# Optimization experiments

Hardware: AMD Instinct MI355X
Metric: run time of the kernel (lower is better)

The kernel has to match this reference:

```python
import jax, jax.numpy as jnp
import numpy as np

B, N_LOCAL, N_GLOBAL, N_PLANE = 8, 512, 512, 512
LQ, LK, NUM_HEADS = 8192, 8192, 8


def setup_inputs() -> dict:
    key = jax.random.key(0)
    ks = jax.random.split(key, 6)
    s = 1.0 / np.sqrt(N_PLANE).astype(np.float32)
    return {
        "x_local": jax.random.normal(ks[0], (B, N_LOCAL, LQ), jnp.float32),
        "x_global": jax.random.normal(ks[1], (B, N_GLOBAL, LK), jnp.float32),
        "Wq": jax.random.normal(ks[2], (N_PLANE, N_LOCAL), jnp.float32) * s,
        "Wk": jax.random.normal(ks[3], (N_PLANE, N_GLOBAL), jnp.float32) * s,
        "Wv": jax.random.normal(ks[4], (N_PLANE, N_GLOBAL), jnp.float32) * s,
        "Wo": jax.random.normal(ks[5], (N_LOCAL, N_PLANE), jnp.float32) * s,
    }


def reference(x_local, x_global, Wq, Wk, Wv, Wo):
    # 1x1 Conv1d (bias=False) == channel-wise GEMM.
    b, _, lq = x_local.shape
    lk = x_global.shape[2]
    h = NUM_HEADS
    d = Wq.shape[0] // h  # d_k = n_plane // num_heads

    # project and split heads: [B, L, P] -> [B, H, L, d]
    q = jnp.einsum('pc,bcl->blp', Wq, x_local).reshape(b, lq, h, d).transpose(0, 2, 1, 3)
    k = jnp.einsum('pc,bcl->blp', Wk, x_global).reshape(b, lk, h, d).transpose(0, 2, 1, 3)
    v = jnp.einsum('pc,bcl->blp', Wv, x_global).reshape(b, lk, h, d).transpose(0, 2, 1, 3)

    # No softmax between QK^T and V -> reassociate: (Q @ K^T) @ V == Q @ (K^T @ V).
    # Avoids the O(Lq*Lk) logits tensor; mathematically identical.
    kv = jnp.einsum('bhkd,bhke->bhde', k, v)          # [B, H, d, d]
    out = jnp.einsum('bhld,bhde->bhle', q, kv) / d     # scale by d_k (as in source)

    # merge heads: [B, H, Lq, d] -> [B, Lq, P] -> output 1x1 conv -> [B, n_local, Lq]
    out = out.transpose(0, 2, 1, 3).reshape(b, lq, h * d)
    return jnp.einsum('op,blp->bol', Wo, out)
```

## Files before the change

kernel.cpp:

```cpp
#include <hip/hip_runtime.h>
#include <stdint.h>


typedef __attribute__((ext_vector_type(8))) short bf16x8;
typedef __attribute__((ext_vector_type(4))) float f32x4;

__device__ __forceinline__ short f2bf(float f) {
  union { float f; uint32_t u; } v; v.f = f;
  uint32_t r = v.u + 0x7FFFu + ((v.u >> 16) & 1u);
  return (short)(r >> 16);
}

__device__ __forceinline__ void async_ld16(const void* g, void* l) {
  __builtin_amdgcn_global_load_lds(
      (const __attribute__((address_space(1))) void*)g,
      (__attribute__((address_space(3))) void*)l, 16, 0, 0);
}

__launch_bounds__(256)
__global__ void prep_weights(const float* __restrict__ Wq, const float* __restrict__ Wk,
                             const float* __restrict__ Wv, const float* __restrict__ Wo,
                             short* __restrict__ Wqt, short* __restrict__ Wkb,
                             short* __restrict__ Wvb, short* __restrict__ Wob) {
  int i = blockIdx.x * 256 + threadIdx.x;
  Wkb[i] = f2bf(Wk[i]);
  Wvb[i] = f2bf(Wv[i]);
  Wob[i] = f2bf(Wo[i]);
  int c = i >> 9, p = i & 511;
  Wqt[i] = f2bf(Wq[p * 512 + c]);
}

__launch_bounds__(256)
__global__ void transpose_cast(const float* __restrict__ X, short* __restrict__ Xt) {
  __shared__ float tile[64][65];
  const int b = blockIdx.z;
  const int l0 = blockIdx.x * 64, c0 = blockIdx.y * 64;
  const int tx = threadIdx.x & 63, ty = threadIdx.x >> 6;
  const float* Xb = X + (size_t)b * 512 * 8192;
  short* Xtb = Xt + (size_t)b * 512 * 8192;
#pragma unroll
  for (int i = 0; i < 16; i++) {
    int c = ty * 16 + i;
    tile[c][tx] = Xb[(size_t)(c0 + c) * 8192 + l0 + tx];
  }
  __syncthreads();
#pragma unroll
  for (int i = 0; i < 16; i++) {
    int l = ty * 16 + i;
    Xtb[(size_t)(l0 + l) * 512 + c0 + tx] = f2bf(tile[tx][l]);
  }
}

template <bool OUT_BF16, bool A_BATCH>
__launch_bounds__(256)
__global__ void gemm_bt(const short* __restrict__ A, const short* __restrict__ B,
                        void* __restrict__ C, int M, int N, int K) {
  __shared__ __align__(16) short As[128 * 32];
  __shared__ __align__(16) short Bs[128 * 32];
  const int tid = threadIdx.x;
  const int lane = tid & 63;
  const int w = tid >> 6;
  const int wy = w >> 1, wx = w & 1;
  const int m0 = blockIdx.y * 128, n0 = blockIdx.x * 128;
  const size_t b = blockIdx.z;
  const short* Ab = A + (A_BATCH ? b * (size_t)M * K : (size_t)0);
  const short* Bb = B + b * (size_t)N * K;
  const int fr = lane & 15, fkg = lane >> 4;

  f32x4 acc[4][4] = {};

  for (int kk = 0; kk < K; kk += 32) {
    __syncthreads();
#pragma unroll
    for (int j = 0; j < 2; j++) {
      int ci = j * 256 + w * 64 + lane;
      int row = ci >> 2;
      int co = (ci & 3) * 8;
      async_ld16(Ab + (size_t)(m0 + row) * K + kk + co, &As[(j * 256 + w * 64) * 8]);
      async_ld16(Bb + (size_t)(n0 + row) * K + kk + co, &Bs[(j * 256 + w * 64) * 8]);
    }
    __syncthreads();

    bf16x8 af[4], bf[4];
#pragma unroll
    for (int t = 0; t < 4; t++) {
      af[t] = *(const bf16x8*)&As[(wy * 64 + t * 16 + fr) * 32 + fkg * 8];
      bf[t] = *(const bf16x8*)&Bs[(wx * 64 + t * 16 + fr) * 32 + fkg * 8];
    }
#pragma unroll
    for (int mt = 0; mt < 4; mt++)
#pragma unroll
      for (int nt = 0; nt < 4; nt++)
        acc[mt][nt] =
            __builtin_amdgcn_mfma_f32_16x16x32_bf16(af[mt], bf[nt], acc[mt][nt], 0, 0, 0);
  }

  const size_t cbase = b * (size_t)M * N;
#pragma unroll
  for (int mt = 0; mt < 4; mt++) {
#pragma unroll
    for (int nt = 0; nt < 4; nt++) {
      int n = n0 + wx * 64 + nt * 16 + fr;
#pragma unroll
      for (int r = 0; r < 4; r++) {
        int m = m0 + wy * 64 + mt * 16 + fkg * 4 + r;
        float v = acc[mt][nt][r];
        if (OUT_BF16)
          ((short*)C)[cbase + (size_t)m * N + n] = f2bf(v);
        else
          ((float*)C)[cbase + (size_t)m * N + n] = v;
      }
    }
  }
}

__launch_bounds__(256)
__global__ void kv_accum(const short* __restrict__ Kb, const short* __restrict__ Vb,
                         float* __restrict__ kv) {
  const int lane = threadIdx.x & 63, w = threadIdx.x >> 6;
  const int b = blockIdx.z, h = blockIdx.y;
  const int l0 = blockIdx.x * 2048 + w * 512;
  const short* Kh = Kb + ((size_t)b * 512 + h * 64) * 8192 + l0;
  const short* Vh = Vb + ((size_t)b * 512 + h * 64) * 8192 + l0;
  const int fr = lane & 15, fkg = lane >> 4;
  f32x4 acc[4][4] = {};
  for (int kk = 0; kk < 512; kk += 32) {
    bf16x8 af[4], bf[4];
#pragma unroll
    for (int t = 0; t < 4; t++) {
      af[t] = *(const bf16x8*)&Kh[(size_t)(t * 16 + fr) * 8192 + kk + fkg * 8];
      bf[t] = *(const bf16x8*)&Vh[(size_t)(t * 16 + fr) * 8192 + kk + fkg * 8];
    }
#pragma unroll
    for (int mt = 0; mt < 4; mt++)
#pragma unroll
      for (int nt = 0; nt < 4; nt++)
        acc[mt][nt] =
            __builtin_amdgcn_mfma_f32_16x16x32_bf16(af[mt], bf[nt], acc[mt][nt], 0, 0, 0);
  }
  float* kvb = kv + ((size_t)b * 8 + h) * 4096;
#pragma unroll
  for (int mt = 0; mt < 4; mt++)
#pragma unroll
    for (int nt = 0; nt < 4; nt++)
#pragma unroll
      for (int r = 0; r < 4; r++) {
        int d = mt * 16 + fkg * 4 + r, e = nt * 16 + fr;
        atomicAdd(&kvb[d * 64 + e], acc[mt][nt][r]);
      }
}

__launch_bounds__(256)
__global__ void u_compute(const float* __restrict__ kv, const short* __restrict__ Wqt,
                          short* __restrict__ Ut) {
  const int lane = threadIdx.x & 63, w = threadIdx.x >> 6;
  const int h = blockIdx.x, b = blockIdx.y;
  const float* kvb = kv + ((size_t)b * 8 + h) * 4096;
  const int fr = lane & 15, fkg = lane >> 4;
  f32x4 acc[4][8] = {};
#pragma unroll
  for (int ks = 0; ks < 2; ks++) {
    bf16x8 af[4];
#pragma unroll
    for (int mt = 0; mt < 4; mt++) {
      union { short s[8]; bf16x8 v; } u;
#pragma unroll
      for (int j = 0; j < 8; j++) {
        int d = ks * 32 + fkg * 8 + j;
        int e = mt * 16 + fr;
        u.s[j] = f2bf(kvb[d * 64 + e] * 0.015625f);
      }
      af[mt] = u.v;
    }
#pragma unroll
    for (int nt = 0; nt < 8; nt++) {
      int c = w * 128 + nt * 16 + fr;
      bf16x8 bfr = *(const bf16x8*)&Wqt[(size_t)c * 512 + h * 64 + ks * 32 + fkg * 8];
#pragma unroll
      for (int mt = 0; mt < 4; mt++)
        acc[mt][nt] =
            __builtin_amdgcn_mfma_f32_16x16x32_bf16(af[mt], bfr, acc[mt][nt], 0, 0, 0);
    }
  }
  short* Utb = Ut + (size_t)b * 262144;
#pragma unroll
  for (int mt = 0; mt < 4; mt++)
#pragma unroll
    for (int nt = 0; nt < 8; nt++) {
      int c = w * 128 + nt * 16 + fr;
#pragma unroll
      for (int r = 0; r < 4; r++) {
        int e = mt * 16 + fkg * 4 + r;
        Utb[(size_t)c * 512 + h * 64 + e] = f2bf(acc[mt][nt][r]);
      }
    }
}

extern "C" void kernel_launch(void* const* d_in, const int* in_sizes, int n_in,
                              void* d_out, int out_size, void* d_ws, size_t ws_size,
                              hipStream_t stream) {
  const float* x_local  = (const float*)d_in[0];
  const float* x_global = (const float*)d_in[1];
  const float* Wq = (const float*)d_in[2];
  const float* Wk = (const float*)d_in[3];
  const float* Wv = (const float*)d_in[4];
  const float* Wo = (const float*)d_in[5];

  char* ws = (char*)d_ws;
  short* Xt  = (short*)(ws + 0);
  float* kv  = (float*)(ws + 67108864);
  short* Ut  = (short*)(ws + 68157440);
  short* Mb  = (short*)(ws + 72351744);
  short* Wkb = (short*)(ws + 76546048);
  short* Wvb = (short*)(ws + 77070336);
  short* Wob = (short*)(ws + 77594624);
  short* Wqt = (short*)(ws + 78118912);

  short* Kb = (short*)d_out;
  short* Vb = (short*)((char*)d_out + 67108864);

  prep_weights<<<1024, 256, 0, stream>>>(Wq, Wk, Wv, Wo, Wqt, Wkb, Wvb, Wob);
  hipMemsetAsync(kv, 0, 1048576, stream);

  transpose_cast<<<dim3(128, 8, 8), 256, 0, stream>>>(x_global, Xt);
  gemm_bt<true, false><<<dim3(64, 4, 8), 256, 0, stream>>>(Wkb, Xt, Kb, 512, 8192, 512);
  gemm_bt<true, false><<<dim3(64, 4, 8), 256, 0, stream>>>(Wvb, Xt, Vb, 512, 8192, 512);

  kv_accum<<<dim3(4, 8, 8), 256, 0, stream>>>(Kb, Vb, kv);
  u_compute<<<dim3(8, 8), 256, 0, stream>>>(kv, Wqt, Ut);
  gemm_bt<true, false><<<dim3(4, 4, 8), 256, 0, stream>>>(Wob, Ut, Mb, 512, 512, 512);

  transpose_cast<<<dim3(128, 8, 8), 256, 0, stream>>>(x_local, Xt);
  gemm_bt<false, true><<<dim3(64, 4, 8), 256, 0, stream>>>(Mb, Xt, d_out, 512, 8192, 512);
}
```

Baseline: 546.5 us.

## Replace K/V projections with Gram matrix of x_global and small weight products

Instead of projecting x_global into full K and V tensors and then reducing K^T V, the code computes the Gram matrix X X^T per batch (split over L and reduced), then forms Wv·G·Wk^T per head via small GEMMs. This removes two large 512x8192 projection GEMMs and their bf16 write/read traffic, as well as the atomics. It needs a partial-sum buffer and a reduction pass, and it adds extra bf16 rounding on the Gram matrix, which may change accuracy.

```diff
diff --git a/kernel.cpp b/kernel.cpp
--- a/kernel.cpp
+++ b/kernel.cpp
@@ -28,6 +28,17 @@
   Wob[i] = f2bf(Wo[i]);
   int c = i >> 9, p = i & 511;
   Wqt[i] = f2bf(Wq[p * 512 + c]);
+}
+
+__launch_bounds__(256)
+__global__ void cast_bf16(const float* __restrict__ X, short* __restrict__ Y) {
+  size_t i = ((size_t)blockIdx.x * 256 + threadIdx.x) * 8;
+  float4 a = *(const float4*)(X + i);
+  float4 b = *(const float4*)(X + i + 4);
+  union { short s[8]; bf16x8 v; } u;
+  u.s[0] = f2bf(a.x); u.s[1] = f2bf(a.y); u.s[2] = f2bf(a.z); u.s[3] = f2bf(a.w);
+  u.s[4] = f2bf(b.x); u.s[5] = f2bf(b.y); u.s[6] = f2bf(b.z); u.s[7] = f2bf(b.w);
+  *(bf16x8*)(Y + i) = u.v;
 }
 
 __launch_bounds__(256)
@@ -115,21 +126,93 @@
 }
 
 __launch_bounds__(256)
-__global__ void kv_accum(const short* __restrict__ Kb, const short* __restrict__ Vb,
-                         float* __restrict__ kv) {
-  const int lane = threadIdx.x & 63, w = threadIdx.x >> 6;
-  const int b = blockIdx.z, h = blockIdx.y;
-  const int l0 = blockIdx.x * 2048 + w * 512;
-  const short* Kh = Kb + ((size_t)b * 512 + h * 64) * 8192 + l0;
-  const short* Vh = Vb + ((size_t)b * 512 + h * 64) * 8192 + l0;
+__global__ void gram_part(const short* __restrict__ X, float* __restrict__ Gp) {
+  __shared__ __align__(16) short As[128 * 32];
+  __shared__ __align__(16) short Bs[128 * 32];
+  const int tid = threadIdx.x;
+  const int lane = tid & 63;
+  const int w = tid >> 6;
+  const int wy = w >> 1, wx = w & 1;
+  const int m0 = blockIdx.y * 128, n0 = blockIdx.x * 128;
+  const int b = blockIdx.z >> 3, s = blockIdx.z & 7;
+  const short* Xb = X + (size_t)b * 512 * 8192;
+  const int k0 = s * 1024;
+  const int fr = lane & 15, fkg = lane >> 4;
+
+  f32x4 acc[4][4] = {};
+
+  for (int kk = k0; kk < k0 + 1024; kk += 32) {
+    __syncthreads();
+#pragma unroll
+    for (int j = 0; j < 2; j++) {
+      int ci = j * 256 + w * 64 + lane;
+      int row = ci >> 2;
+      int co = (ci & 3) * 8;
+      async_ld16(Xb + (size_t)(m0 + row) * 8192 + kk + co, &As[(j * 256 + w * 64) * 8]);
+      async_ld16(Xb + (size_t)(n0 + row) * 8192 + kk + co, &Bs[(j * 256 + w * 64) * 8]);
+    }
+    __syncthreads();
+
+    bf16x8 af[4], bf[4];
+#pragma unroll
+    for (int t = 0; t < 4; t++) {
+      af[t] = *(const bf16x8*)&As[(wy * 64 + t * 16 + fr) * 32 + fkg * 8];
+      bf[t] = *(const bf16x8*)&Bs[(wx * 64 + t * 16 + fr) * 32 + fkg * 8];
+    }
+#pragma unroll
+    for (int mt = 0; mt < 4; mt++)
+#pragma unroll
+      for (int nt = 0; nt < 4; nt++)
+        acc[mt][nt] =
+            __builtin_amdgcn_mfma_f32_16x16x32_bf16(af[mt], bf[nt], acc[mt][nt], 0, 0, 0);
+  }
+
+  float* Gz = Gp + (size_t)blockIdx.z * 262144;
+#pragma unroll
+  for (int mt = 0; mt < 4; mt++)
+#pragma unroll
+    for (int nt = 0; nt < 4; nt++) {
+      int n = n0 + wx * 64 + nt * 16 + fr;
+#pragma unroll
+      for (int r = 0; r < 4; r++) {
+        int m = m0 + wy * 64 + mt * 16 + fkg * 4 + r;
+        Gz[(size_t)m * 512 + n] = acc[mt][nt][r];
+      }
+    }
+}
+
+__launch_bounds__(256)
+__global__ void g_reduce(const float* __restrict__ Gp, short* __restrict__ Gb) {
+  size_t i = ((size_t)blockIdx.x * 256 + threadIdx.x) * 4;
+  int b = (int)(i >> 18);
+  int r = (int)(i & 262143);
+  const float* base = Gp + (size_t)b * 8 * 262144 + r;
+  float4 acc = {0.f, 0.f, 0.f, 0.f};
+#pragma unroll
+  for (int j = 0; j < 8; j++) {
+    float4 t = *(const float4*)(base + (size_t)j * 262144);
+    acc.x += t.x; acc.y += t.y; acc.z += t.z; acc.w += t.w;
+  }
+  union { short s[4]; uint64_t u; } o;
+  o.s[0] = f2bf(acc.x); o.s[1] = f2bf(acc.y); o.s[2] = f2bf(acc.z); o.s[3] = f2bf(acc.w);
+  *(uint64_t*)(Gb + i) = o.u;
+}
+
+__launch_bounds__(64)
+__global__ void r_kernel(const short* __restrict__ Tp, const short* __restrict__ Wkb,
+                         short* __restrict__ Rt) {
+  const int lane = threadIdx.x;
+  const int h = blockIdx.x, b = blockIdx.y;
+  const short* Te = Tp + ((size_t)b * 512 + h * 64) * 512;
+  const short* Wk = Wkb + (size_t)h * 64 * 512;
   const int fr = lane & 15, fkg = lane >> 4;
   f32x4 acc[4][4] = {};
   for (int kk = 0; kk < 512; kk += 32) {
     bf16x8 af[4], bf[4];
 #pragma unroll
     for (int t = 0; t < 4; t++) {
-      af[t] = *(const bf16x8*)&Kh[(size_t)(t * 16 + fr) * 8192 + kk + fkg * 8];
-      bf[t] = *(const bf16x8*)&Vh[(size_t)(t * 16 + fr) * 8192 + kk + fkg * 8];
+      af[t] = *(const bf16x8*)&Te[(size_t)(t * 16 + fr) * 512 + kk + fkg * 8];
+      bf[t] = *(const bf16x8*)&Wk[(size_t)(t * 16 + fr) * 512 + kk + fkg * 8];
     }
 #pragma unroll
     for (int mt = 0; mt < 4; mt++)
@@ -138,40 +221,33 @@
         acc[mt][nt] =
             __builtin_amdgcn_mfma_f32_16x16x32_bf16(af[mt], bf[nt], acc[mt][nt], 0, 0, 0);
   }
-  float* kvb = kv + ((size_t)b * 8 + h) * 4096;
+  short* Rh = Rt + ((size_t)b * 8 + h) * 4096;
 #pragma unroll
   for (int mt = 0; mt < 4; mt++)
 #pragma unroll
     for (int nt = 0; nt < 4; nt++)
 #pragma unroll
       for (int r = 0; r < 4; r++) {
-        int d = mt * 16 + fkg * 4 + r, e = nt * 16 + fr;
-        atomicAdd(&kvb[d * 64 + e], acc[mt][nt][r]);
+        int e = mt * 16 + fkg * 4 + r;
+        int d = nt * 16 + fr;
+        Rh[e * 64 + d] = f2bf(acc[mt][nt][r] * 0.015625f);
       }
 }
 
 __launch_bounds__(256)
-__global__ void u_compute(const float* __restrict__ kv, const short* __restrict__ Wqt,
+__global__ void u_compute(const short* __restrict__ Rt, const short* __restrict__ Wqt,
                           short* __restrict__ Ut) {
   const int lane = threadIdx.x & 63, w = threadIdx.x >> 6;
   const int h = blockIdx.x, b = blockIdx.y;
-  const float* kvb = kv + ((size_t)b * 8 + h) * 4096;
+  const short* Rh = Rt + ((size_t)b * 8 + h) * 4096;
   const int fr = lane & 15, fkg = lane >> 4;
   f32x4 acc[4][8] = {};
 #pragma unroll
   for (int ks = 0; ks < 2; ks++) {
     bf16x8 af[4];
 #pragma unroll
-    for (int mt = 0; mt < 4; mt++) {
-      union { short s[8]; bf16x8 v; } u;
-#pragma unroll
-      for (int j = 0; j < 8; j++) {
-        int d = ks * 32 + fkg * 8 + j;
-        int e = mt * 16 + fr;
-        u.s[j] = f2bf(kvb[d * 64 + e] * 0.015625f);
-      }
-      af[mt] = u.v;
-    }
+    for (int mt = 0; mt < 4; mt++)
+      af[mt] = *(const bf16x8*)&Rh[(mt * 16 + fr) * 64 + ks * 32 + fkg * 8];
 #pragma unroll
     for (int nt = 0; nt < 8; nt++) {
       int c = w * 128 + nt * 16 + fr;
@@ -207,29 +283,32 @@
   const float* Wo = (const float*)d_in[5];
 
   char* ws = (char*)d_ws;
-  short* Xt  = (short*)(ws + 0);
-  float* kv  = (float*)(ws + 67108864);
-  short* Ut  = (short*)(ws + 68157440);
-  short* Mb  = (short*)(ws + 72351744);
-  short* Wkb = (short*)(ws + 76546048);
-  short* Wvb = (short*)(ws + 77070336);
-  short* Wob = (short*)(ws + 77594624);
-  short* Wqt = (short*)(ws + 78118912);
-
-  short* Kb = (short*)d_out;
-  short* Vb = (short*)((char*)d_out + 67108864);
+  short* Xlt = (short*)(ws + 0);
+  short* Rt  = (short*)(ws + 67108864);
+  short* Ut  = (short*)(ws + 67633152);
+  short* Mb  = (short*)(ws + 71827456);
+  short* Wkb = (short*)(ws + 76021760);
+  short* Wvb = (short*)(ws + 76546048);
+  short* Wob = (short*)(ws + 77070336);
+  short* Wqt = (short*)(ws + 77594624);
+
+  short* Xgb   = (short*)d_out;
+  float* Gpart = (float*)((char*)d_out + 67108864);
+  short* Gb    = (short*)d_out;
+  short* Tp    = (short*)((char*)d_out + 4194304);
 
   prep_weights<<<1024, 256, 0, stream>>>(Wq, Wk, Wv, Wo, Wqt, Wkb, Wvb, Wob);
-  hipMemsetAsync(kv, 0, 1048576, stream);
-
-  transpose_cast<<<dim3(128, 8, 8), 256, 0, stream>>>(x_global, Xt);
-  gemm_bt<true, false><<<dim3(64, 4, 8), 256, 0, stream>>>(Wkb, Xt, Kb, 512, 8192, 512);
-  gemm_bt<true, false><<<dim3(64, 4, 8), 256, 0, stream>>>(Wvb, Xt, Vb, 512, 8192, 512);
-
-  kv_accum<<<dim3(4, 8, 8), 256, 0, stream>>>(Kb, Vb, kv);
-  u_compute<<<dim3(8, 8), 256, 0, stream>>>(kv, Wqt, Ut);
+
+  transpose_cast<<<dim3(128, 8, 8), 256, 0, stream>>>(x_local, Xlt);
+
+  cast_bf16<<<16384, 256, 0, stream>>>(x_global, Xgb);
+  gram_part<<<dim3(4, 4, 64), 256, 0, stream>>>(Xgb, Gpart);
+  g_reduce<<<2048, 256, 0, stream>>>(Gpart, Gb);
+
+  gemm_bt<true, false><<<dim3(4, 4, 8), 256, 0, stream>>>(Wvb, Gb, Tp, 512, 512, 512);
+  r_kernel<<<dim3(8, 8), 64, 0, stream>>>(Tp, Wkb, Rt);
+  u_compute<<<dim3(8, 8), 256, 0, stream>>>(Rt, Wqt, Ut);
   gemm_bt<true, false><<<dim3(4, 4, 8), 256, 0, stream>>>(Wob, Ut, Mb, 512, 512, 512);
 
-  transpose_cast<<<dim3(128, 8, 8), 256, 0, stream>>>(x_local, Xt);
-  gemm_bt<false, true><<<dim3(64, 4, 8), 256, 0, stream>>>(Mb, Xt, d_out, 512, 8192, 512);
-}
+  gemm_bt<false, true><<<dim3(64, 4, 8), 256, 0, stream>>>(Mb, Xlt, d_out, 512, 8192, 512);
+}
```

After: 516.7 us. -5.5%, faster.
